# Optimization experiments

Hardware: AMD Instinct MI355X
Metric: run time of the kernel (lower is better)

## Reference

```python
import jax, jax.numpy as jnp
import numpy as np

EPS = 1e-6


def setup_inputs() -> dict:
    key = jax.random.key(0)
    ks = jax.random.split(key, 10)
    N1, N2, K, E, LAYERS = 4096, 4096, 10, 262144, 3
    D = 2 ** K  # 1024
    us = jax.random.uniform(ks[0], (LAYERS, N1, D), dtype=jnp.float32)
    vs = jax.random.uniform(ks[1], (LAYERS, N2, D), dtype=jnp.float32)
    gamma = jax.random.normal(ks[2], (N1, LAYERS), dtype=jnp.float32)
    delta = jax.random.normal(ks[3], (N2, LAYERS), dtype=jnp.float32)
    latent_z1 = jax.random.uniform(ks[4], (N1, LAYERS), dtype=jnp.float32)
    latent_w1 = jax.random.uniform(ks[5], (N2, LAYERS), dtype=jnp.float32)
    # p_k_l initialized as log(uniform) in torch; any real values are valid params
    p_ks = jnp.full((LAYERS, K + 1), jnp.log(1.0 / (K + 1)), dtype=jnp.float32)
    p_ks = p_ks + 0.01 * jax.random.normal(ks[6], (LAYERS, K + 1), dtype=jnp.float32)
    L_ = 5.0 * jnp.ones((1,), dtype=jnp.float32)
    sparse_is = jax.random.randint(ks[7], (LAYERS, E), 0, N1, dtype=jnp.int64) if jax.config.jax_enable_x64 else jax.random.randint(ks[7], (LAYERS, E), 0, N1).astype(jnp.int32)
    sparse_js = jax.random.randint(ks[8], (LAYERS, E), 0, N2).astype(sparse_is.dtype)
    return {"us": us, "vs": vs, "gamma": gamma, "delta": delta,
            "latent_z1": latent_z1, "latent_w1": latent_w1,
            "p_ks": p_ks, "L_": L_,
            "sparse_is": sparse_is, "sparse_js": sparse_js}


def reference(us, vs, gamma, delta, latent_z1, latent_w1, p_ks, L_, sparse_is, sparse_js):
    LAYERS, N1, D = us.shape
    N2 = vs.shape[1]
    K = p_ks.shape[1] - 1  # tree_height
    latent_z = jax.nn.softmax(latent_z1, axis=1)  # Softmax(dim=1)
    latent_w = jax.nn.softmax(latent_w1, axis=1)
    L = jax.nn.softplus(L_)[0]
    ll = jnp.float32(0.0)
    for layer in range(LAYERS):
        p_k = jax.nn.softmax(p_ks[layer], axis=0)  # soft_0
        g = gamma[:, layer]                         # [N1]
        d = delta[:, layer]                         # [N2]
        emb_z = jax.nn.softmax(us[layer], axis=1)   # [N1, D]
        emb_w = jax.nn.softmax(vs[layer], axis=1)   # [N2, D]
        # hierarchical tree-weighted similarity: sum of GEMMs at coarsening levels
        inter = p_k[0] * jnp.ones((N1, N2), dtype=us.dtype)
        z_k, w_k = emb_z, emb_w
        for k in range(1, K):
            z_k = z_k.reshape(N1, -1, 2).sum(axis=2)  # [N1, D/2^k]
            w_k = w_k.reshape(N2, -1, 2).sum(axis=2)  # [N2, D/2^k]
            inter = inter + p_k[k] * jnp.einsum('nd,md->nm', z_k, w_k + EPS)
        inter = inter + p_k[K] * jnp.einsum('nd,md->nm', emb_z, emb_w + EPS)
        mat_1 = g[:, None] + d[None, :]                              # [N1, N2]
        mat_0 = (latent_z[:, layer][:, None] * L) * (latent_w[:, layer] + EPS)[None, :] * inter
        mat = jax.nn.softplus(mat_0 + mat_1)
        z_pdist1 = mat.sum()
        if N1 == N2:  # remove diagonal contributions
            z_pdist1 = z_pdist1 - jnp.trace(mat)
        i_ = sparse_is[layer]
        j_ = sparse_js[layer]
        z_pdist2 = (mat_0[i_, j_] + mat_1[i_, j_]).sum()
        ll = ll + (z_pdist2 - z_pdist1)
    return ll
```

## Files before the change

kernel.cpp:

```cpp
#include <hip/hip_runtime.h>
#include <hip/hip_bf16.h>
#include <stdint.h>

#define EPSV 1e-6f
#define N1 4096
#define N2 4096
#define DD 1024
#define NLAYERS 3
#define KKC 10

typedef __bf16 bf16_t;
typedef __bf16 bf16x8 __attribute__((ext_vector_type(8)));
typedef float f32x4 __attribute__((ext_vector_type(4)));
typedef long longx2 __attribute__((ext_vector_type(2)));

#define ZSCALE 256.0f
#define WSCALE 64.0f
#define INVSCALE 6.103515625e-05f

__device__ __forceinline__ float softplus_fast(float x) {
  return fmaxf(x, 0.f) + __logf(1.f + __expf(-fabsf(x)));
}
__device__ __forceinline__ float softplus_ref(float x) {
  return fmaxf(x, 0.f) + log1pf(expf(-fabsf(x)));
}
__device__ __forceinline__ float wredsum(float x) {
  #pragma unroll
  for (int o = 32; o; o >>= 1) x += __shfl_xor(x, o, 64);
  return x;
}
__device__ __forceinline__ float wredmax(float x) {
  #pragma unroll
  for (int o = 32; o; o >>= 1) x = fmaxf(x, __shfl_xor(x, o, 64));
  return x;
}
__device__ __forceinline__ void global_load_lds16(const void* g, void* l) {
  __builtin_amdgcn_global_load_lds(
      (const __attribute__((address_space(1))) uint32_t*)g,
      (__attribute__((address_space(3))) uint32_t*)l, 16, 0, 0);
}

__device__ __forceinline__ uint32_t enc_e4m3(float x) {
  if (x < 0.015625f) return (uint32_t)__float2int_rn(x * 512.0f);
  uint32_t u = __float_as_uint(x);
  u += 0x7FFFFu + ((u >> 20) & 1u);
  return (((u >> 23) - 120u) << 3) | ((u >> 20) & 7u);
}

__global__ __launch_bounds__(256) void prep_small(
    const float* __restrict__ lz, const float* __restrict__ lw,
    const float* __restrict__ gamma, const float* __restrict__ delta,
    const float* __restrict__ pks, const float* __restrict__ Lp,
    float* __restrict__ consts, float* __restrict__ a_tab, float* __restrict__ b_tab,
    float* __restrict__ g_tab, float* __restrict__ d_tab,
    uint32_t* __restrict__ hist, float* __restrict__ out)
{
  int n = blockIdx.x * blockDim.x + threadIdx.x;
  float Lv = softplus_ref(Lp[0]);
  if (n == 0) out[0] = 0.f;
  if (n < NLAYERS*256) hist[n] = 0u;
  if (n < N1) {
    float z0 = lz[n*3], z1 = lz[n*3+1], z2 = lz[n*3+2];
    float m = fmaxf(z0, fmaxf(z1, z2));
    float e0 = expf(z0-m), e1 = expf(z1-m), e2 = expf(z2-m);
    float inv = 1.f/(e0+e1+e2);
    a_tab[0*N1+n] = e0*inv*Lv; a_tab[1*N1+n] = e1*inv*Lv; a_tab[2*N1+n] = e2*inv*Lv;
    float w0 = lw[n*3], w1 = lw[n*3+1], w2 = lw[n*3+2];
    m = fmaxf(w0, fmaxf(w1, w2));
    e0 = expf(w0-m); e1 = expf(w1-m); e2 = expf(w2-m);
    inv = 1.f/(e0+e1+e2);
    b_tab[0*N2+n] = e0*inv+EPSV; b_tab[1*N2+n] = e1*inv+EPSV; b_tab[2*N2+n] = e2*inv+EPSV;
    #pragma unroll
    for (int k = 0; k < 3; ++k) {
      g_tab[k*N1+n] = gamma[n*3+k];
      d_tab[k*N2+n] = delta[n*3+k];
    }
  }
  if (n < NLAYERS) {
    float p[KKC+1]; float m = -1e30f;
    for (int k = 0; k <= KKC; ++k) { p[k] = pks[n*(KKC+1)+k]; m = fmaxf(m, p[k]); }
    float s = 0.f;
    for (int k = 0; k <= KKC; ++k) { p[k] = expf(p[k]-m); s += p[k]; }
    float inv = 1.f/s;
    for (int k = 0; k <= KKC; ++k) consts[8 + n*(KKC+1) + k] = p[k]*inv;
    consts[n] = p[0]*inv + EPSV*(1.f - p[0]*inv);
  }
}

#define EPB 2048

__global__ __launch_bounds__(256) void edge_hist(
    const int* __restrict__ is_, const int* __restrict__ js_,
    uint32_t* __restrict__ hist, int E)
{
  __shared__ uint32_t h[256];
  const int lay = blockIdx.y;
  const int t = threadIdx.x;
  h[t] = 0u;
  __syncthreads();
  const int e0 = blockIdx.x * EPB;
  const int e1 = min(e0 + EPB, E);
  for (int e = e0 + t; e < e1; e += 256) {
    int i = is_[(size_t)lay*E + e], j = js_[(size_t)lay*E + e];
    atomicAdd(&h[(i>>8)*16 + (j>>8)], 1u);
  }
  __syncthreads();
  if (h[t]) atomicAdd(&hist[lay*256 + t], h[t]);
}

__global__ __launch_bounds__(256) void edge_scan(
    const uint32_t* __restrict__ hist, uint32_t* __restrict__ off,
    uint32_t* __restrict__ cursor)
{
  __shared__ uint32_t sa[768], sb[768];
  const int t = threadIdx.x;
  for (int i = t; i < 768; i += 256) sa[i] = hist[i];
  __syncthreads();
  uint32_t* src = sa; uint32_t* dst = sb;
  for (int s = 1; s < 768; s <<= 1) {
    for (int i = t; i < 768; i += 256) dst[i] = src[i] + (i >= s ? src[i-s] : 0u);
    __syncthreads();
    uint32_t* tmp = src; src = dst; dst = tmp;
  }
  for (int i = t; i < 768; i += 256) {
    uint32_t ex = i ? src[i-1] : 0u;
    off[i] = ex; cursor[i] = ex;
  }
  if (t == 0) off[768] = src[767];
}

__global__ __launch_bounds__(256) void edge_scatter(
    const int* __restrict__ is_, const int* __restrict__ js_,
    uint32_t* __restrict__ cursor, uint16_t* __restrict__ ebuf, int E)
{
  __shared__ uint32_t h[256];
  __shared__ uint32_t basev[256];
  const int lay = blockIdx.y;
  const int t = threadIdx.x;
  h[t] = 0u;
  __syncthreads();
  const int e0 = blockIdx.x * EPB;
  const int e1 = min(e0 + EPB, E);
  for (int e = e0 + t; e < e1; e += 256) {
    int i = is_[(size_t)lay*E + e], j = js_[(size_t)lay*E + e];
    atomicAdd(&h[(i>>8)*16 + (j>>8)], 1u);
  }
  __syncthreads();
  basev[t] = h[t] ? atomicAdd(&cursor[lay*256 + t], h[t]) : 0u;
  h[t] = 0u;
  __syncthreads();
  for (int e = e0 + t; e < e1; e += 256) {
    int i = is_[(size_t)lay*E + e], j = js_[(size_t)lay*E + e];
    int b = (i>>8)*16 + (j>>8);
    uint32_t r = atomicAdd(&h[b], 1u);
    ebuf[basev[b] + r] = (uint16_t)(((i & 255) << 8) | (j & 255));
  }
}

__global__ __launch_bounds__(256) void prep_rows(
    const float* __restrict__ us, const float* __restrict__ vs,
    uint8_t* __restrict__ zt8, uint8_t* __restrict__ wt8, size_t lstride,
    const float* __restrict__ consts, int layer0)
{
  const int t = threadIdx.x, w = t >> 6, l = t & 63;
  const int n = blockIdx.x*4 + w;
  const int layer = layer0 + blockIdx.y;
  const int zmode = (blockIdx.z == 0);
  const float* src = (zmode ? us : vs) + ((size_t)layer*N1 + n)*DD + l*16;
  uint8_t* drow = (zmode ? zt8 : wt8) + (size_t)blockIdx.y*lstride + (size_t)n*1024;
  const int p0 = (l>>2)*64 + ((l&1)*2)*16 + ((l&3)>>1)*8;

  float e[16];
  {
    const float4* s4 = (const float4*)src;
    float4 u0 = s4[0], u1 = s4[1], u2 = s4[2], u3 = s4[3];
    e[0]=u0.x; e[1]=u0.y; e[2]=u0.z; e[3]=u0.w;
    e[4]=u1.x; e[5]=u1.y; e[6]=u1.z; e[7]=u1.w;
    e[8]=u2.x; e[9]=u2.y; e[10]=u2.z; e[11]=u2.w;
    e[12]=u3.x; e[13]=u3.y; e[14]=u3.z; e[15]=u3.w;
  }
  float mx = e[0];
  #pragma unroll
  for (int i = 1; i < 16; ++i) mx = fmaxf(mx, e[i]);
  mx = wredmax(mx);
  float s = 0.f;
  #pragma unroll
  for (int i = 0; i < 16; ++i) { e[i] = __expf(e[i]-mx); s += e[i]; }
  s = wredsum(s);
  float inv = 1.f/s;
  #pragma unroll
  for (int i = 0; i < 16; ++i) e[i] *= inv;

  uint32_t b4[4] = {0u, 0u, 0u, 0u};
  if (!zmode) {
    #pragma unroll
    for (int i = 0; i < 16; ++i)
      b4[i>>2] |= enc_e4m3(e[i]*WSCALE) << ((i&3)*8);
  } else {
    float s1[8], s2[4], s3[2], s4v;
    #pragma unroll
    for (int i = 0; i < 8; ++i) s1[i] = e[2*i] + e[2*i+1];
    #pragma unroll
    for (int i = 0; i < 4; ++i) s2[i] = s1[2*i] + s1[2*i+1];
    s3[0] = s2[0]+s2[1]; s3[1] = s2[2]+s2[3];
    s4v = s3[0]+s3[1];
    float s5 = s4v + __shfl_xor(s4v, 1, 64);
    float s6 = s5  + __shfl_xor(s5, 2, 64);
    float s7 = s6  + __shfl_xor(s6, 4, 64);
    float s8 = s7  + __shfl_xor(s7, 8, 64);
    float s9 = s8  + __shfl_xor(s8, 16, 64);
    const float* pk = consts + 8 + layer*(KKC+1);
    const float base = pk[4]*s4v + pk[5]*s5 + pk[6]*s6 + pk[7]*s7 + pk[8]*s8 + pk[9]*s9;
    const float p1 = pk[1], p2 = pk[2], p3 = pk[3], p10 = pk[10];
    #pragma unroll
    for (int i = 0; i < 16; ++i) {
      float v = p10*e[i] + p1*s1[i>>1] + p2*s2[i>>2] + p3*s3[i>>3] + base;
      b4[i>>2] |= enc_e4m3(v*ZSCALE) << ((i&3)*8);
    }
  }
  uint64_t u0 = (uint64_t)b4[0] | ((uint64_t)b4[1] << 32);
  uint64_t u1 = (uint64_t)b4[2] | ((uint64_t)b4[3] << 32);
  *(uint64_t*)(drow + p0)      = u0;
  *(uint64_t*)(drow + p0 + 16) = u1;
}

__global__ __launch_bounds__(512, 2) void gemm_fused(
    const uint8_t* __restrict__ Az8, size_t zls,
    const uint8_t* __restrict__ Bw8, size_t wls,
    const float* __restrict__ a_tab, const float* __restrict__ b_tab,
    const float* __restrict__ g_tab, const float* __restrict__ d_tab,
    const float* __restrict__ consts, int layer0,
    const uint32_t* __restrict__ eoff, const uint16_t* __restrict__ ebuf,
    float* __restrict__ out)
{
  extern __shared__ char lds[];
  const int t = threadIdx.x;
  const int w = t >> 6, l = t & 63;
  const int wm = w >> 2, wn = w & 3;
  const int fr = l & 15, fq = l >> 4;

  const int nbx = gridDim.x, nby = gridDim.y;
  int lid = blockIdx.x + nbx*(blockIdx.y + nby*blockIdx.z);
  const int nblk = nbx*nby*gridDim.z;
  const int cpx = nblk >> 3;
  int nid = (lid & 7)*cpx + (lid >> 3);
  const int bz = nid / (nbx*nby);
  const int rem = nid % (nbx*nby);
  const int bi = rem % nbx, bj = rem / nbx;

  const int i0 = bi*256, j0 = bj*256;
  const int layer = layer0 + bz;
  Az8 += (size_t)bz*zls + (size_t)i0*1024;
  Bw8 += (size_t)bz*wls + (size_t)j0*1024;

  f32x4 acc[8][4];
  f32x4 zero = {0.f, 0.f, 0.f, 0.f};
  #pragma unroll
  for (int m = 0; m < 8; ++m)
    #pragma unroll
    for (int nn = 0; nn < 4; ++nn) acc[m][nn] = zero;

  const int go = (l & 7) ^ (l >> 3);
  const size_t s_off = (size_t)((l >> 3)*2 + (go >> 2))*1024 + (size_t)(go & 3)*16;
  const int sl = fr >> 1;
  const int slot = (((fr & 1) << 2) + fq) ^ sl;
  const int abase = wm*8192 + sl*128 + slot*16;
  const int bbase = 16384 + wn*4096 + sl*128 + slot*16;

  longx2 ar2[4], br2[4];

#define STG_A(tile) do { \
    char* _d = lds + ((tile)&3)*32768 + w*2048; \
    const uint8_t* _s = Az8 + (size_t)(w*32)*1024 + (size_t)(tile)*64 + s_off; \
    global_load_lds16(_s, _d); \
    global_load_lds16(_s + (size_t)16*1024, _d + 1024); \
  } while (0)
#define STG_B(tile) do { \
    char* _d = lds + ((tile)&3)*32768 + 16384 + w*2048; \
    const uint8_t* _s = Bw8 + (size_t)(w*32)*1024 + (size_t)(tile)*64 + s_off; \
    global_load_lds16(_s, _d); \
    global_load_lds16(_s + (size_t)16*1024, _d + 1024); \
  } while (0)
#define LDA(bufb, mq) do { \
    const char* _b = lds + (bufb) + abase; \
    _Pragma("unroll") for (int i = 0; i < 4; ++i) \
      ar2[i] = *(const longx2*)(_b + ((mq)*4+i)*1024); \
  } while (0)
#define LDB(bufb, nq) do { \
    const char* _b = lds + (bufb) + bbase; \
    _Pragma("unroll") for (int j = 0; j < 2; ++j) \
      br2[(nq)*2+j] = *(const longx2*)(_b + ((nq)*2+j)*1024); \
  } while (0)
#define MM(mq, nq) do { \
    _Pragma("unroll") for (int i = 0; i < 4; ++i) \
    _Pragma("unroll") for (int j = 0; j < 2; ++j) { \
      acc[(mq)*4+i][(nq)*2+j] = __builtin_amdgcn_mfma_f32_16x16x32_fp8_fp8( \
          ar2[i].x, br2[(nq)*2+j].x, acc[(mq)*4+i][(nq)*2+j], 0, 0, 0); \
      acc[(mq)*4+i][(nq)*2+j] = __builtin_amdgcn_mfma_f32_16x16x32_fp8_fp8( \
          ar2[i].y, br2[(nq)*2+j].y, acc[(mq)*4+i][(nq)*2+j], 0, 0, 0); } \
  } while (0)
#define BAR() asm volatile("s_barrier" ::: "memory")
#define PRIO_MM(mq, nq) do { \
    __builtin_amdgcn_s_setprio(1); MM(mq, nq); __builtin_amdgcn_s_setprio(0); } while (0)

  STG_A(0); STG_B(0); STG_A(1); STG_B(1);
  asm volatile("s_waitcnt vmcnt(4)" ::: "memory");
  BAR();

  #pragma unroll 4
  for (int u = 0; u < 16; ++u) {
    const int cb = (u & 3)*32768;
    LDA(cb, 0); LDB(cb, 0);
    if (u < 14) STG_A(u+2);
    BAR(); PRIO_MM(0, 0);
    LDB(cb, 1);
    if (u < 14) STG_B(u+2);
    BAR(); PRIO_MM(0, 1);
    LDA(cb, 1);
    BAR(); PRIO_MM(1, 0);
    if (u < 14)       asm volatile("s_waitcnt vmcnt(4)" ::: "memory");
    else if (u == 14) asm volatile("s_waitcnt vmcnt(0)" ::: "memory");
    BAR(); PRIO_MM(1, 1);
  }
#undef STG_A
#undef STG_B
#undef LDA
#undef LDB
#undef MM
#undef BAR
#undef PRIO_MM

  const float cc = consts[layer];
  {
    char* cbase = lds + wm*65536 + fq*2048 + wn*128 + fr*2;
    #pragma unroll
    for (int m = 0; m < 8; ++m)
      #pragma unroll
      for (int nn = 0; nn < 4; ++nn)
        #pragma unroll
        for (int r = 0; r < 4; ++r)
          *(bf16_t*)(cbase + m*8192 + r*512 + nn*32) =
              (bf16_t)(acc[m][nn][r]*INVSCALE + cc);
  }
  __syncthreads();

  const float* at = a_tab + layer*N1;
  const float* bt = b_tab + layer*N2;
  const float* gt = g_tab + layer*N1;
  const float* dt = d_tab + layer*N2;
  float dsum = 0.f;
  #pragma unroll 4
  for (int i = 0; i < 16; ++i) {
    const int id = t + i*512;
    const int row = id >> 5, g = id & 31;
    bf16x8 v = *(const bf16x8*)(lds + row*512 + g*16);
    const int grow = i0 + row, gcol = j0 + g*8;
    const float av = at[grow], gv = gt[grow];
    float4 b0 = *(const float4*)(bt + gcol), b1 = *(const float4*)(bt + gcol + 4);
    float4 d0 = *(const float4*)(dt + gcol), d1 = *(const float4*)(dt + gcol + 4);
    float bb[8] = {b0.x,b0.y,b0.z,b0.w,b1.x,b1.y,b1.z,b1.w};
    float dd[8] = {d0.x,d0.y,d0.z,d0.w,d1.x,d1.y,d1.z,d1.w};
    #pragma unroll
    for (int e2 = 0; e2 < 8; ++e2) {
      float x = av*bb[e2]*(float)v[e2] + gv + dd[e2];
      float sp = softplus_fast(x);
      dsum += (grow != gcol + e2) ? sp : 0.f;
    }
  }
  const int bin = bz*256 + bi*16 + bj;
  const uint32_t e0 = eoff[bin], e1 = eoff[bin+1];
  float ssum = 0.f;
  for (uint32_t e = e0 + (uint32_t)t; e < e1; e += 512u) {
    const int pk2 = ebuf[e];
    const int li = pk2 >> 8, lj = pk2 & 255;
    float dc = (float)*(const bf16_t*)(lds + li*512 + lj*2);
    ssum += at[i0+li]*bt[j0+lj]*dc + gt[i0+li] + dt[j0+lj];
  }
  float tot = wredsum(ssum - dsum);
  __syncthreads();
  if (l == 0) ((float*)lds)[w] = tot;
  __syncthreads();
  if (t == 0) {
    const float* r = (const float*)lds;
    float s = 0.f;
    #pragma unroll
    for (int i = 0; i < 8; ++i) s += r[i];
    atomicAdd(out, s);
  }
}

extern "C" void kernel_launch(void* const* d_in, const int* in_sizes, int n_in,
                              void* d_out, int out_size, void* d_ws, size_t ws_size,
                              hipStream_t stream) {
  const float* us    = (const float*)d_in[0];
  const float* vs    = (const float*)d_in[1];
  const float* gamma = (const float*)d_in[2];
  const float* delta = (const float*)d_in[3];
  const float* lz    = (const float*)d_in[4];
  const float* lw    = (const float*)d_in[5];
  const float* pks   = (const float*)d_in[6];
  const float* Lp    = (const float*)d_in[7];
  const int*   sis   = (const int*)d_in[8];
  const int*   sjs   = (const int*)d_in[9];
  float* out = (float*)d_out;
  char*  ws  = (char*)d_ws;
  const int E = in_sizes[8] / NLAYERS;

  size_t p = 0;
  float* consts = (float*)(ws + p); p += 1024;
  float* a_tab  = (float*)(ws + p); p += (size_t)NLAYERS*N1*4;
  float* b_tab  = (float*)(ws + p); p += (size_t)NLAYERS*N2*4;
  float* g_tab  = (float*)(ws + p); p += (size_t)NLAYERS*N1*4;
  float* d_tab  = (float*)(ws + p); p += (size_t)NLAYERS*N2*4;
  uint32_t* hist   = (uint32_t*)(ws + p); p += 1024*4;
  uint32_t* eoff   = (uint32_t*)(ws + p); p += 1024*4;
  uint32_t* cursor = (uint32_t*)(ws + p); p += 1024*4;
  uint16_t* ebuf   = (uint16_t*)(ws + p); p += (size_t)NLAYERS*E*2;
  p = (p + 4095) & ~(size_t)4095;
  uint8_t* zt8 = (uint8_t*)(ws + p); p += (size_t)NLAYERS*N1*1024;
  uint8_t* wt8 = (uint8_t*)(ws + p); p += (size_t)NLAYERS*N2*1024;
  if (ws_size < p) return;
  const size_t ZLS = (size_t)N1*1024;
  const size_t LDSB = 131072;
  const int nebl = (E + EPB - 1) / EPB;

  prep_small<<<(N1+255)/256, 256, 0, stream>>>(lz, lw, gamma, delta, pks, Lp,
                                               consts, a_tab, b_tab, g_tab, d_tab,
                                               hist, out);
  edge_hist<<<dim3(nebl, NLAYERS), 256, 0, stream>>>(sis, sjs, hist, E);
  edge_scan<<<1, 256, 0, stream>>>(hist, eoff, cursor);
  edge_scatter<<<dim3(nebl, NLAYERS), 256, 0, stream>>>(sis, sjs, cursor, ebuf, E);
  prep_rows<<<dim3(N1/4, NLAYERS, 2), 256, 0, stream>>>(us, vs, zt8, wt8, ZLS, consts, 0);
  gemm_fused<<<dim3(16,16,NLAYERS), 512, LDSB, stream>>>(
      zt8, ZLS, wt8, ZLS, a_tab, b_tab, g_tab, d_tab, consts, 0, eoff, ebuf, out);
}
```

Measured before the change: 151.8 us.

## Halve GEMM row tile to 128 with double-buffered loop and finer edge bins

Changes the fused FP8 GEMM block tile from 256x256 to 128x256, doubling the grid to 32x16x3 blocks and shrinking LDS to 64KB so more blocks fit per CU (launch bounds raised to 4). The four-stage LDS pipeline with interleaved barriers and split MFMA phases is replaced by a simpler two-buffer loop that waits for all loads each iteration. Edge binning is refined to 128-row bins (512 bins per layer) so sparse edges match the new tiles. This trades B-operand reuse and deep prefetch for more parallelism and occupancy; the full vmcnt(0) wait each step may expose memory latency.

```diff
diff --git a/kernel.cpp b/kernel.cpp
--- a/kernel.cpp
+++ b/kernel.cpp
@@ -17,6 +17,9 @@
 #define ZSCALE 256.0f
 #define WSCALE 64.0f
 #define INVSCALE 6.103515625e-05f
+
+#define NBIN_L 512
+#define NBIN_T (NLAYERS*NBIN_L)
 
 __device__ __forceinline__ float softplus_fast(float x) {
   return fmaxf(x, 0.f) + __logf(1.f + __expf(-fabsf(x)));
@@ -58,7 +61,7 @@
   int n = blockIdx.x * blockDim.x + threadIdx.x;
   float Lv = softplus_ref(Lp[0]);
   if (n == 0) out[0] = 0.f;
-  if (n < NLAYERS*256) hist[n] = 0u;
+  if (n < NBIN_T) hist[n] = 0u;
   if (n < N1) {
     float z0 = lz[n*3], z1 = lz[n*3+1], z2 = lz[n*3+2];
     float m = fmaxf(z0, fmaxf(z1, z2));
@@ -93,67 +96,69 @@
     const int* __restrict__ is_, const int* __restrict__ js_,
     uint32_t* __restrict__ hist, int E)
 {
-  __shared__ uint32_t h[256];
+  __shared__ uint32_t h[NBIN_L];
   const int lay = blockIdx.y;
   const int t = threadIdx.x;
-  h[t] = 0u;
+  h[t] = 0u; h[t+256] = 0u;
   __syncthreads();
   const int e0 = blockIdx.x * EPB;
   const int e1 = min(e0 + EPB, E);
   for (int e = e0 + t; e < e1; e += 256) {
     int i = is_[(size_t)lay*E + e], j = js_[(size_t)lay*E + e];
-    atomicAdd(&h[(i>>8)*16 + (j>>8)], 1u);
-  }
-  __syncthreads();
-  if (h[t]) atomicAdd(&hist[lay*256 + t], h[t]);
+    atomicAdd(&h[(i>>7)*16 + (j>>8)], 1u);
+  }
+  __syncthreads();
+  if (h[t])     atomicAdd(&hist[lay*NBIN_L + t], h[t]);
+  if (h[t+256]) atomicAdd(&hist[lay*NBIN_L + t + 256], h[t+256]);
 }
 
 __global__ __launch_bounds__(256) void edge_scan(
     const uint32_t* __restrict__ hist, uint32_t* __restrict__ off,
     uint32_t* __restrict__ cursor)
 {
-  __shared__ uint32_t sa[768], sb[768];
+  __shared__ uint32_t sa[NBIN_T], sb[NBIN_T];
   const int t = threadIdx.x;
-  for (int i = t; i < 768; i += 256) sa[i] = hist[i];
+  for (int i = t; i < NBIN_T; i += 256) sa[i] = hist[i];
   __syncthreads();
   uint32_t* src = sa; uint32_t* dst = sb;
-  for (int s = 1; s < 768; s <<= 1) {
-    for (int i = t; i < 768; i += 256) dst[i] = src[i] + (i >= s ? src[i-s] : 0u);
+  for (int s = 1; s < NBIN_T; s <<= 1) {
+    for (int i = t; i < NBIN_T; i += 256) dst[i] = src[i] + (i >= s ? src[i-s] : 0u);
     __syncthreads();
     uint32_t* tmp = src; src = dst; dst = tmp;
   }
-  for (int i = t; i < 768; i += 256) {
+  for (int i = t; i < NBIN_T; i += 256) {
     uint32_t ex = i ? src[i-1] : 0u;
     off[i] = ex; cursor[i] = ex;
   }
-  if (t == 0) off[768] = src[767];
+  if (t == 0) off[NBIN_T] = src[NBIN_T-1];
 }
 
 __global__ __launch_bounds__(256) void edge_scatter(
     const int* __restrict__ is_, const int* __restrict__ js_,
     uint32_t* __restrict__ cursor, uint16_t* __restrict__ ebuf, int E)
 {
-  __shared__ uint32_t h[256];
-  __shared__ uint32_t basev[256];
+  __shared__ uint32_t h[NBIN_L];
+  __shared__ uint32_t basev[NBIN_L];
   const int lay = blockIdx.y;
   const int t = threadIdx.x;
-  h[t] = 0u;
+  h[t] = 0u; h[t+256] = 0u;
   __syncthreads();
   const int e0 = blockIdx.x * EPB;
   const int e1 = min(e0 + EPB, E);
   for (int e = e0 + t; e < e1; e += 256) {
     int i = is_[(size_t)lay*E + e], j = js_[(size_t)lay*E + e];
-    atomicAdd(&h[(i>>8)*16 + (j>>8)], 1u);
-  }
-  __syncthreads();
-  basev[t] = h[t] ? atomicAdd(&cursor[lay*256 + t], h[t]) : 0u;
-  h[t] = 0u;
+    atomicAdd(&h[(i>>7)*16 + (j>>8)], 1u);
+  }
+  __syncthreads();
+  basev[t]     = h[t]     ? atomicAdd(&cursor[lay*NBIN_L + t], h[t]) : 0u;
+  basev[t+256] = h[t+256] ? atomicAdd(&cursor[lay*NBIN_L + t + 256], h[t+256]) : 0u;
+  h[t] = 0u; h[t+256] = 0u;
   __syncthreads();
   for (int e = e0 + t; e < e1; e += 256) {
     int i = is_[(size_t)lay*E + e], j = js_[(size_t)lay*E + e];
-    int b = (i>>8)*16 + (j>>8);
+    int b = (i>>7)*16 + (j>>8);
     uint32_t r = atomicAdd(&h[b], 1u);
-    ebuf[basev[b] + r] = (uint16_t)(((i & 255) << 8) | (j & 255));
+    ebuf[basev[b] + r] = (uint16_t)(((i & 127) << 8) | (j & 255));
   }
 }
 
@@ -224,7 +229,7 @@
   *(uint64_t*)(drow + p0 + 16) = u1;
 }
 
-__global__ __launch_bounds__(512, 2) void gemm_fused(
+__global__ __launch_bounds__(512, 4) void gemm_fused(
     const uint8_t* __restrict__ Az8, size_t zls,
     const uint8_t* __restrict__ Bw8, size_t wls,
     const float* __restrict__ a_tab, const float* __restrict__ b_tab,
@@ -248,93 +253,72 @@
   const int rem = nid % (nbx*nby);
   const int bi = rem % nbx, bj = rem / nbx;
 
-  const int i0 = bi*256, j0 = bj*256;
+  const int i0 = bi*128, j0 = bj*256;
   const int layer = layer0 + bz;
   Az8 += (size_t)bz*zls + (size_t)i0*1024;
   Bw8 += (size_t)bz*wls + (size_t)j0*1024;
 
-  f32x4 acc[8][4];
+  f32x4 acc[4][4];
   f32x4 zero = {0.f, 0.f, 0.f, 0.f};
   #pragma unroll
-  for (int m = 0; m < 8; ++m)
+  for (int m = 0; m < 4; ++m)
     #pragma unroll
     for (int nn = 0; nn < 4; ++nn) acc[m][nn] = zero;
 
   const int go = (l & 7) ^ (l >> 3);
   const size_t s_off = (size_t)((l >> 3)*2 + (go >> 2))*1024 + (size_t)(go & 3)*16;
-  const int sl = fr >> 1;
-  const int slot = (((fr & 1) << 2) + fq) ^ sl;
-  const int abase = wm*8192 + sl*128 + slot*16;
-  const int bbase = 16384 + wn*4096 + sl*128 + slot*16;
+  const int slot = (((fr & 1) << 2) + fq) ^ (fr >> 1);
+  const int abase = wm*4096 + (fr>>1)*128 + slot*16;
+  const int bbase = 8192 + wn*4096 + (fr>>1)*128 + slot*16;
 
   longx2 ar2[4], br2[4];
 
 #define STG_A(tile) do { \
-    char* _d = lds + ((tile)&3)*32768 + w*2048; \
-    const uint8_t* _s = Az8 + (size_t)(w*32)*1024 + (size_t)(tile)*64 + s_off; \
+    char* _d = lds + ((tile)&1)*24576 + w*1024; \
+    const uint8_t* _s = Az8 + (size_t)(w*16)*1024 + (size_t)(tile)*64 + s_off; \
     global_load_lds16(_s, _d); \
-    global_load_lds16(_s + (size_t)16*1024, _d + 1024); \
   } while (0)
 #define STG_B(tile) do { \
-    char* _d = lds + ((tile)&3)*32768 + 16384 + w*2048; \
+    char* _d = lds + ((tile)&1)*24576 + 8192 + w*2048; \
     const uint8_t* _s = Bw8 + (size_t)(w*32)*1024 + (size_t)(tile)*64 + s_off; \
     global_load_lds16(_s, _d); \
     global_load_lds16(_s + (size_t)16*1024, _d + 1024); \
   } while (0)
-#define LDA(bufb, mq) do { \
-    const char* _b = lds + (bufb) + abase; \
-    _Pragma("unroll") for (int i = 0; i < 4; ++i) \
-      ar2[i] = *(const longx2*)(_b + ((mq)*4+i)*1024); \
-  } while (0)
-#define LDB(bufb, nq) do { \
-    const char* _b = lds + (bufb) + bbase; \
-    _Pragma("unroll") for (int j = 0; j < 2; ++j) \
-      br2[(nq)*2+j] = *(const longx2*)(_b + ((nq)*2+j)*1024); \
-  } while (0)
-#define MM(mq, nq) do { \
-    _Pragma("unroll") for (int i = 0; i < 4; ++i) \
-    _Pragma("unroll") for (int j = 0; j < 2; ++j) { \
-      acc[(mq)*4+i][(nq)*2+j] = __builtin_amdgcn_mfma_f32_16x16x32_fp8_fp8( \
-          ar2[i].x, br2[(nq)*2+j].x, acc[(mq)*4+i][(nq)*2+j], 0, 0, 0); \
-      acc[(mq)*4+i][(nq)*2+j] = __builtin_amdgcn_mfma_f32_16x16x32_fp8_fp8( \
-          ar2[i].y, br2[(nq)*2+j].y, acc[(mq)*4+i][(nq)*2+j], 0, 0, 0); } \
-  } while (0)
-#define BAR() asm volatile("s_barrier" ::: "memory")
-#define PRIO_MM(mq, nq) do { \
-    __builtin_amdgcn_s_setprio(1); MM(mq, nq); __builtin_amdgcn_s_setprio(0); } while (0)
-
-  STG_A(0); STG_B(0); STG_A(1); STG_B(1);
-  asm volatile("s_waitcnt vmcnt(4)" ::: "memory");
-  BAR();
-
-  #pragma unroll 4
+
+  STG_A(0); STG_B(0);
+
   for (int u = 0; u < 16; ++u) {
-    const int cb = (u & 3)*32768;
-    LDA(cb, 0); LDB(cb, 0);
-    if (u < 14) STG_A(u+2);
-    BAR(); PRIO_MM(0, 0);
-    LDB(cb, 1);
-    if (u < 14) STG_B(u+2);
-    BAR(); PRIO_MM(0, 1);
-    LDA(cb, 1);
-    BAR(); PRIO_MM(1, 0);
-    if (u < 14)       asm volatile("s_waitcnt vmcnt(4)" ::: "memory");
-    else if (u == 14) asm volatile("s_waitcnt vmcnt(0)" ::: "memory");
-    BAR(); PRIO_MM(1, 1);
+    const int cb = (u & 1)*24576;
+    asm volatile("s_waitcnt vmcnt(0)" ::: "memory");
+    asm volatile("s_barrier" ::: "memory");
+    #pragma unroll
+    for (int i = 0; i < 4; ++i)
+      ar2[i] = *(const longx2*)(lds + cb + abase + i*1024);
+    #pragma unroll
+    for (int j = 0; j < 4; ++j)
+      br2[j] = *(const longx2*)(lds + cb + bbase + j*1024);
+    if (u < 15) { STG_A(u+1); STG_B(u+1); }
+    __builtin_amdgcn_s_setprio(1);
+    #pragma unroll
+    for (int i = 0; i < 4; ++i)
+      #pragma unroll
+      for (int j = 0; j < 4; ++j) {
+        acc[i][j] = __builtin_amdgcn_mfma_f32_16x16x32_fp8_fp8(
+            ar2[i].x, br2[j].x, acc[i][j], 0, 0, 0);
+        acc[i][j] = __builtin_amdgcn_mfma_f32_16x16x32_fp8_fp8(
+            ar2[i].y, br2[j].y, acc[i][j], 0, 0, 0);
+      }
+    __builtin_amdgcn_s_setprio(0);
   }
 #undef STG_A
 #undef STG_B
-#undef LDA
-#undef LDB
-#undef MM
-#undef BAR
-#undef PRIO_MM
-
+
+  __syncthreads();
   const float cc = consts[layer];
   {
-    char* cbase = lds + wm*65536 + fq*2048 + wn*128 + fr*2;
-    #pragma unroll
-    for (int m = 0; m < 8; ++m)
+    char* cbase = lds + wm*32768 + fq*2048 + wn*128 + fr*2;
+    #pragma unroll
+    for (int m = 0; m < 4; ++m)
       #pragma unroll
       for (int nn = 0; nn < 4; ++nn)
         #pragma unroll
@@ -350,7 +334,7 @@
   const float* dt = d_tab + layer*N2;
   float dsum = 0.f;
   #pragma unroll 4
-  for (int i = 0; i < 16; ++i) {
+  for (int i = 0; i < 8; ++i) {
     const int id = t + i*512;
     const int row = id >> 5, g = id & 31;
     bf16x8 v = *(const bf16x8*)(lds + row*512 + g*16);
@@ -367,7 +351,7 @@
       dsum += (grow != gcol + e2) ? sp : 0.f;
     }
   }
-  const int bin = bz*256 + bi*16 + bj;
+  const int bin = bz*NBIN_L + bi*16 + bj;
   const uint32_t e0 = eoff[bin], e1 = eoff[bin+1];
   float ssum = 0.f;
   for (uint32_t e = e0 + (uint32_t)t; e < e1; e += 512u) {
@@ -412,16 +396,16 @@
   float* b_tab  = (float*)(ws + p); p += (size_t)NLAYERS*N2*4;
   float* g_tab  = (float*)(ws + p); p += (size_t)NLAYERS*N1*4;
   float* d_tab  = (float*)(ws + p); p += (size_t)NLAYERS*N2*4;
-  uint32_t* hist   = (uint32_t*)(ws + p); p += 1024*4;
-  uint32_t* eoff   = (uint32_t*)(ws + p); p += 1024*4;
-  uint32_t* cursor = (uint32_t*)(ws + p); p += 1024*4;
+  uint32_t* hist   = (uint32_t*)(ws + p); p += 2048*4;
+  uint32_t* eoff   = (uint32_t*)(ws + p); p += 2048*4;
+  uint32_t* cursor = (uint32_t*)(ws + p); p += 2048*4;
   uint16_t* ebuf   = (uint16_t*)(ws + p); p += (size_t)NLAYERS*E*2;
   p = (p + 4095) & ~(size_t)4095;
   uint8_t* zt8 = (uint8_t*)(ws + p); p += (size_t)NLAYERS*N1*1024;
   uint8_t* wt8 = (uint8_t*)(ws + p); p += (size_t)NLAYERS*N2*1024;
   if (ws_size < p) return;
   const size_t ZLS = (size_t)N1*1024;
-  const size_t LDSB = 131072;
+  const size_t LDSB = 65536;
   const int nebl = (E + EPB - 1) / EPB;
 
   prep_small<<<(N1+255)/256, 256, 0, stream>>>(lz, lw, gamma, delta, pks, Lp,
@@ -431,6 +415,6 @@
   edge_scan<<<1, 256, 0, stream>>>(hist, eoff, cursor);
   edge_scatter<<<dim3(nebl, NLAYERS), 256, 0, stream>>>(sis, sjs, cursor, ebuf, E);
   prep_rows<<<dim3(N1/4, NLAYERS, 2), 256, 0, stream>>>(us, vs, zt8, wt8, ZLS, consts, 0);
-  gemm_fused<<<dim3(16,16,NLAYERS), 512, LDSB, stream>>>(
+  gemm_fused<<<dim3(32,16,NLAYERS), 512, LDSB, stream>>>(
       zt8, ZLS, wt8, ZLS, a_tab, b_tab, g_tab, d_tab, consts, 0, eoff, ebuf, out);
 }
```

Result: faster. 139.6 us (median of 2 runs) (-8.1%).
